# Performance work log

Hardware: AMD Instinct MI355X
Metric: run time of the kernel (lower is better)

Reference implementation:

```python
import jax, jax.numpy as jnp
import numpy as np

B, S, D = 8, 2048, 512  # batch, seq_len, dim_val == dim_attn

def setup_inputs() -> dict:
    key = jax.random.key(0)
    kx, kq, kk, kv = jax.random.split(key, 4)
    scale = 1.0 / np.sqrt(D)
    return {
        "x": jax.random.normal(kx, (B, S, D), dtype=jnp.float32),
        "Wq": jax.random.normal(kq, (D, D), dtype=jnp.float32) * scale,  # dim_input -> dim_attn
        "Wk": jax.random.normal(kk, (D, D), dtype=jnp.float32) * scale,
        "Wv": jax.random.normal(kv, (D, D), dtype=jnp.float32) * scale,  # dim_input -> dim_val
    }

def reference(x, Wq, Wk, Wv):
    # bias-free linear projections (nn.Linear stores W as [out,in]; here W is [in,out])
    Q = jnp.einsum("bsd,de->bse", x, Wq)
    K = jnp.einsum("bsd,de->bse", x, Wk)
    V = jnp.einsum("bsd,de->bse", x, Wv)
    # manual scaled dot-product attention: softmax(QK^T / sqrt(d_attn)) V
    scores = jnp.einsum("bqe,bke->bqk", Q, K) / jnp.sqrt(jnp.asarray(Q.shape[-1], Q.dtype))
    a = jax.nn.softmax(scores, axis=-1)
    return jnp.einsum("bqk,bkd->bqd", a, V)
```

## Files before the change

### kernel.cpp

```cpp
#include <hip/hip_runtime.h>


typedef __attribute__((ext_vector_type(8))) short bf16x8;
typedef __attribute__((ext_vector_type(4))) float f32x4;

__device__ __forceinline__ short f2bf(float f) {
  union { float f; unsigned u; } v; v.f = f;
  unsigned r = v.u + 0x7fffu + ((v.u >> 16) & 1u);
  return (short)(r >> 16);
}

__device__ __forceinline__ void async_cp16(const void* g, void* l) {
  __builtin_amdgcn_global_load_lds(
      (const __attribute__((address_space(1))) unsigned int*)g,
      (__attribute__((address_space(3))) unsigned int*)l, 16, 0, 0);
}

__global__ __launch_bounds__(256) void prep_kernel(const float* __restrict__ x,
                                                   const float* __restrict__ Wq,
                                                   const float* __restrict__ Wk,
                                                   const float* __restrict__ Wv,
                                                   short* __restrict__ WT,
                                                   short* __restrict__ xb) {
  if (blockIdx.x < 384) {
    int g = blockIdx.x * 256 + threadIdx.x;
    int w = g >> 15;
    int rem = g & 32767;
    int n = rem & 511;
    int k0 = (rem >> 9) << 3;
    const float* W = (w == 0) ? Wq : ((w == 1) ? Wk : Wv);
    bf16x8 o;
#pragma unroll
    for (int j = 0; j < 8; ++j) o[j] = f2bf(W[(k0 + j) * 512 + n]);
    *(bf16x8*)(WT + w * 262144 + n * 512 + k0) = o;
  } else {
    size_t g = (size_t)(blockIdx.x - 384) * 256 + threadIdx.x;
    size_t off = g * 8;
    f32x4 lo = *(const f32x4*)(x + off);
    f32x4 hi = *(const f32x4*)(x + off + 4);
    bf16x8 o;
    o[0] = f2bf(lo[0]); o[1] = f2bf(lo[1]); o[2] = f2bf(lo[2]); o[3] = f2bf(lo[3]);
    o[4] = f2bf(hi[0]); o[5] = f2bf(hi[1]); o[6] = f2bf(hi[2]); o[7] = f2bf(hi[3]);
    *(bf16x8*)(xb + off) = o;
  }
}

__global__ __launch_bounds__(256) void proj_kernel(const short* __restrict__ xb,
                                                   const short* __restrict__ WT,
                                                   short* __restrict__ QP,
                                                   short* __restrict__ KP,
                                                   short* __restrict__ VP) {
  __shared__ __align__(16) short smem[128 * 136];
  short* Af = smem;
  short* Bf = smem + 4096;
  short* Tb = smem;

  const int tid = threadIdx.x, wv = tid >> 6, ln = tid & 63;
  const int lane_m = ln & 15, lane_q = ln >> 4;
  const int z = blockIdx.z;
  const int m0 = blockIdx.x * 128, n0 = blockIdx.y * 128;
  const short* WTz = WT + z * 262144;
  const int wm = wv & 1, wn = wv >> 1;

  f32x4 zero4 = {0.f, 0.f, 0.f, 0.f};
  f32x4 acc[4][4];
#pragma unroll
  for (int i = 0; i < 4; ++i)
#pragma unroll
    for (int j = 0; j < 4; ++j) acc[i][j] = zero4;

#pragma unroll 1
  for (int kk = 0; kk < 16; ++kk) {
    const int k0 = kk * 32;
    __syncthreads();
#pragma unroll
    for (int i = 0; i < 2; ++i) {
      const int mt = wv * 2 + i;
      async_cp16(xb + (size_t)(m0 + mt * 16 + lane_m) * 512 + k0 + lane_q * 8, Af + mt * 512);
      async_cp16(WTz + (n0 + mt * 16 + lane_m) * 512 + k0 + lane_q * 8, Bf + mt * 512);
    }
    __syncthreads();
    bf16x8 a[4], b[4];
#pragma unroll
    for (int i = 0; i < 4; ++i) a[i] = *(bf16x8*)(Af + ((wm * 4 + i) * 64 + ln) * 8);
#pragma unroll
    for (int j = 0; j < 4; ++j) b[j] = *(bf16x8*)(Bf + ((wn * 4 + j) * 64 + ln) * 8);
#pragma unroll
    for (int i = 0; i < 4; ++i)
#pragma unroll
      for (int j = 0; j < 4; ++j)
        acc[i][j] = __builtin_amdgcn_mfma_f32_16x16x32_bf16(a[i], b[j], acc[i][j], 0, 0, 0);
  }
  __syncthreads();

  const int bb = m0 >> 11, ktg = (m0 & 2047) >> 6;
  if (z < 2) {
#pragma unroll
    for (int i = 0; i < 4; ++i)
#pragma unroll
      for (int j = 0; j < 4; ++j)
#pragma unroll
        for (int rr = 0; rr < 4; ++rr)
          Tb[(wm * 64 + i * 16 + lane_q * 4 + rr) * 136 + wn * 64 + j * 16 + lane_m] = f2bf(acc[i][j][rr]);
    __syncthreads();
    short* O = (z == 0) ? QP : KP;
    const int ksg0 = n0 >> 5;
#pragma unroll
    for (int p = 0; p < 8; ++p) {
      const int c2 = p * 256 + tid;
      const int ktl = c2 >> 10, wvv = (c2 >> 8) & 3, ksl = (c2 >> 6) & 3;
      const int lq = (c2 >> 4) & 3, lm = c2 & 15;
      const short* src = Tb + (ktl * 64 + wvv * 16 + lm) * 136 + ksl * 32 + lq * 8;
      size_t chunk = (size_t)bb * 131072 + (size_t)(ktg + ktl) * 4096 + wvv * 1024 +
                     (ksg0 + ksl) * 64 + lq * 16 + lm;
      *(bf16x8*)(O + chunk * 8) = *(const bf16x8*)src;
    }
  } else {
#pragma unroll
    for (int i = 0; i < 4; ++i)
#pragma unroll
      for (int j = 0; j < 4; ++j)
#pragma unroll
        for (int rr = 0; rr < 4; ++rr) {
          int rl = wm * 64 + i * 16 + lane_q * 4 + rr;
          int cl = wn * 64 + j * 16 + lane_m;
          Tb[cl * 136 + rl] = f2bf(acc[i][j][rr]);
        }
    __syncthreads();
    const int wvv = n0 >> 7;
#pragma unroll
    for (int p = 0; p < 8; ++p) {
      const int c2 = p * 256 + tid;
      const int ktl = c2 >> 10, nt = (c2 >> 7) & 7, ks2 = (c2 >> 6) & 1;
      const int lq = (c2 >> 4) & 3, lm = c2 & 15;
      const short* src = Tb + (nt * 16 + lm) * 136 + ktl * 64 + ks2 * 32 + lq * 8;
      size_t chunk = (size_t)bb * 131072 + (size_t)(ktg + ktl) * 4096 + wvv * 1024 +
                     nt * 128 + ks2 * 64 + lq * 16 + lm;
      *(bf16x8*)(VP + chunk * 8) = *(const bf16x8*)src;
    }
  }
}


#define ISSUE_K(ka0_, ka1_, ka2_, ka3_)                                      \
  asm volatile("global_load_dwordx4 %0, %16, %20\n\t"                        \
               "global_load_dwordx4 %1, %16, %20 offset:1024\n\t"            \
               "global_load_dwordx4 %2, %16, %20 offset:2048\n\t"            \
               "global_load_dwordx4 %3, %16, %20 offset:3072\n\t"            \
               "global_load_dwordx4 %4, %17, %20\n\t"                        \
               "global_load_dwordx4 %5, %17, %20 offset:1024\n\t"            \
               "global_load_dwordx4 %6, %17, %20 offset:2048\n\t"            \
               "global_load_dwordx4 %7, %17, %20 offset:3072\n\t"            \
               "global_load_dwordx4 %8, %18, %20\n\t"                        \
               "global_load_dwordx4 %9, %18, %20 offset:1024\n\t"            \
               "global_load_dwordx4 %10, %18, %20 offset:2048\n\t"           \
               "global_load_dwordx4 %11, %18, %20 offset:3072\n\t"           \
               "global_load_dwordx4 %12, %19, %20\n\t"                       \
               "global_load_dwordx4 %13, %19, %20 offset:1024\n\t"           \
               "global_load_dwordx4 %14, %19, %20 offset:2048\n\t"           \
               "global_load_dwordx4 %15, %19, %20 offset:3072\n\t"           \
               : "=&v"(kfr[0]), "=&v"(kfr[1]), "=&v"(kfr[2]), "=&v"(kfr[3]), \
                 "=&v"(kfr[4]), "=&v"(kfr[5]), "=&v"(kfr[6]), "=&v"(kfr[7]), \
                 "=&v"(kfr[8]), "=&v"(kfr[9]), "=&v"(kfr[10]), "=&v"(kfr[11]), \
                 "=&v"(kfr[12]), "=&v"(kfr[13]), "=&v"(kfr[14]), "=&v"(kfr[15]) \
               : "v"(ka0_), "v"(ka1_), "v"(ka2_), "v"(ka3_), "s"(Kp))

#define ISSUE_V0(va0_, va1_, va2_, va3_)                                     \
  asm volatile("global_load_dwordx4 %0, %8, %12\n\t"                         \
               "global_load_dwordx4 %1, %8, %12 offset:2048\n\t"             \
               "global_load_dwordx4 %2, %9, %12\n\t"                         \
               "global_load_dwordx4 %3, %9, %12 offset:2048\n\t"             \
               "global_load_dwordx4 %4, %10, %12\n\t"                        \
               "global_load_dwordx4 %5, %10, %12 offset:2048\n\t"            \
               "global_load_dwordx4 %6, %11, %12\n\t"                        \
               "global_load_dwordx4 %7, %11, %12 offset:2048\n\t"            \
               : "=&v"(bvp0[0]), "=&v"(bvp0[1]), "=&v"(bvp0[2]), "=&v"(bvp0[3]), \
                 "=&v"(bvp0[4]), "=&v"(bvp0[5]), "=&v"(bvp0[6]), "=&v"(bvp0[7]) \
               : "v"(va0_), "v"(va1_), "v"(va2_), "v"(va3_), "s"(VTp))

#define ISSUE_V1(va0_, va1_, va2_, va3_)                                     \
  asm volatile("global_load_dwordx4 %0, %8, %12 offset:1024\n\t"             \
               "global_load_dwordx4 %1, %8, %12 offset:3072\n\t"             \
               "global_load_dwordx4 %2, %9, %12 offset:1024\n\t"             \
               "global_load_dwordx4 %3, %9, %12 offset:3072\n\t"             \
               "global_load_dwordx4 %4, %10, %12 offset:1024\n\t"            \
               "global_load_dwordx4 %5, %10, %12 offset:3072\n\t"            \
               "global_load_dwordx4 %6, %11, %12 offset:1024\n\t"            \
               "global_load_dwordx4 %7, %11, %12 offset:3072\n\t"            \
               : "=&v"(bvp1[0]), "=&v"(bvp1[1]), "=&v"(bvp1[2]), "=&v"(bvp1[3]), \
                 "=&v"(bvp1[4]), "=&v"(bvp1[5]), "=&v"(bvp1[6]), "=&v"(bvp1[7]) \
               : "v"(va0_), "v"(va1_), "v"(va2_), "v"(va3_), "s"(VTp))

#define WAITK()                                                              \
  asm volatile("s_waitcnt vmcnt(8)"                                          \
               : "+v"(kfr[0]), "+v"(kfr[1]), "+v"(kfr[2]), "+v"(kfr[3]),     \
                 "+v"(kfr[4]), "+v"(kfr[5]), "+v"(kfr[6]), "+v"(kfr[7]),     \
                 "+v"(kfr[8]), "+v"(kfr[9]), "+v"(kfr[10]), "+v"(kfr[11]),   \
                 "+v"(kfr[12]), "+v"(kfr[13]), "+v"(kfr[14]), "+v"(kfr[15]))

#define WAITV()                                                              \
  asm volatile("s_waitcnt vmcnt(0)"                                          \
               : "+v"(bvp0[0]), "+v"(bvp0[1]), "+v"(bvp0[2]), "+v"(bvp0[3]), \
                 "+v"(bvp0[4]), "+v"(bvp0[5]), "+v"(bvp0[6]), "+v"(bvp0[7]), \
                 "+v"(bvp1[0]), "+v"(bvp1[1]), "+v"(bvp1[2]), "+v"(bvp1[3]), \
                 "+v"(bvp1[4]), "+v"(bvp1[5]), "+v"(bvp1[6]), "+v"(bvp1[7]))

#define DRAIN_K()                                                            \
  asm volatile("s_waitcnt vmcnt(0)"                                          \
               : "+v"(kfr[0]), "+v"(kfr[1]), "+v"(kfr[2]), "+v"(kfr[3]),     \
                 "+v"(kfr[4]), "+v"(kfr[5]), "+v"(kfr[6]), "+v"(kfr[7]),     \
                 "+v"(kfr[8]), "+v"(kfr[9]), "+v"(kfr[10]), "+v"(kfr[11]),   \
                 "+v"(kfr[12]), "+v"(kfr[13]), "+v"(kfr[14]), "+v"(kfr[15]))

__global__ __launch_bounds__(256, 2) void flash_kernel(const short* __restrict__ Q,
                                                       const short* __restrict__ K,
                                                       const short* __restrict__ VT,
                                                       float* __restrict__ out) {
  __shared__ __align__(16) short qf[16384];
  __shared__ __align__(16) short pf[4096];
  __shared__ float l_red[4][32];

  const int tid = threadIdx.x, wv = tid >> 6, ln = tid & 63;
  const int lane_m = ln & 15, lane_q = ln >> 4;
  const int b = blockIdx.x & 7, m0 = (blockIdx.x >> 3) * 32;
  const short* Qp = Q + (size_t)b * 1048576;
  const short* Kp = K + (size_t)b * 1048576;
  const short* VTp = VT + (size_t)b * 1048576;
  const float sc2 = 0.044194173824159216f * 1.4426950408889634f;

  {
    const int qt = m0 >> 6, wvm = (m0 >> 4) & 3;
#pragma unroll
    for (int r = 0; r < 8; ++r) {
      const int region = wv * 8 + r;
      const int mi = region & 1, ks = region >> 1;
      const short* src = Qp + ((size_t)(qt * 4096 + (wvm + mi) * 1024 + ks * 64) + ln) * 8;
      *(bf16x8*)(qf + (region * 64 + ln) * 8) = *(const bf16x8*)src;
    }
  }

  f32x4 zero4 = {0.f, 0.f, 0.f, 0.f};
  f32x4 O[2][8];
#pragma unroll
  for (int mi = 0; mi < 2; ++mi)
#pragma unroll
    for (int nt = 0; nt < 8; ++nt) O[mi][nt] = zero4;

  float lp[2][4] = {{0.f, 0.f, 0.f, 0.f}, {0.f, 0.f, 0.f, 0.f}};

  const unsigned kvb = (unsigned)(wv * 16384 + ln * 16);

  const int kstep = wv >> 1;
  const int quad = ((wv & 1) << 1) | (lane_m >> 3);
  const int jj = lane_m & 7;
  const int effr = ln ^ (ln >> 4);

  __syncthreads();

  bf16x8 kfr[16], bvp0[8], bvp1[8];
  ISSUE_K(kvb, kvb + 4096u, kvb + 8192u, kvb + 12288u);

#pragma unroll 1
  for (int kt = 0; kt < 32; ++kt) {
    const unsigned va0 = kvb + (unsigned)(kt * 65536);
    ISSUE_V0(va0, va0 + 4096u, va0 + 8192u, va0 + 12288u);
    WAITK();
    f32x4 s0a = zero4, s0b = zero4, s1a = zero4, s1b = zero4;
#pragma unroll
    for (int ks = 0; ks < 16; ++ks) {
      bf16x8 a0 = *(bf16x8*)(qf + ((ks * 2 + 0) * 64 + ln) * 8);
      bf16x8 a1 = *(bf16x8*)(qf + ((ks * 2 + 1) * 64 + ln) * 8);
      if (ks & 1) {
        s0b = __builtin_amdgcn_mfma_f32_16x16x32_bf16(a0, kfr[ks], s0b, 0, 0, 0);
        s1b = __builtin_amdgcn_mfma_f32_16x16x32_bf16(a1, kfr[ks], s1b, 0, 0, 0);
      } else {
        s0a = __builtin_amdgcn_mfma_f32_16x16x32_bf16(a0, kfr[ks], s0a, 0, 0, 0);
        s1a = __builtin_amdgcn_mfma_f32_16x16x32_bf16(a1, kfr[ks], s1a, 0, 0, 0);
      }
    }
    f32x4 sacc0 = s0a + s0b, sacc1 = s1a + s1b;

    ISSUE_V1(va0, va0 + 4096u, va0 + 8192u, va0 + 12288u);

    short* pfb = pf + (kt & 1) * 2048;
#pragma unroll
    for (int rr = 0; rr < 4; ++rr) {
      const int m = lane_q * 4 + rr;
      const int eff = (m ^ quad) + quad * 16;
      float p0 = exp2f(sacc0[rr] * sc2 - 12.0f);
      float p1 = exp2f(sacc1[rr] * sc2 - 12.0f);
      lp[0][rr] += p0;
      lp[1][rr] += p1;
      pfb[((kstep * 2 + 0) * 64 + eff) * 8 + jj] = f2bf(p0);
      pfb[((kstep * 2 + 1) * 64 + eff) * 8 + jj] = f2bf(p1);
    }
    __syncthreads();

    WAITV();
    bf16x8 a00 = *(bf16x8*)(pfb + (0 * 64 + effr) * 8);
    bf16x8 a01 = *(bf16x8*)(pfb + (1 * 64 + effr) * 8);
#pragma unroll
    for (int nt = 0; nt < 8; ++nt) {
      O[0][nt] = __builtin_amdgcn_mfma_f32_16x16x32_bf16(a00, bvp0[nt], O[0][nt], 0, 0, 0);
      O[1][nt] = __builtin_amdgcn_mfma_f32_16x16x32_bf16(a01, bvp0[nt], O[1][nt], 0, 0, 0);
    }
    {
      const unsigned ka0 = kvb + (unsigned)((((kt + 1) & 31)) * 65536);
      ISSUE_K(ka0, ka0 + 4096u, ka0 + 8192u, ka0 + 12288u);
    }
    bf16x8 a10 = *(bf16x8*)(pfb + (2 * 64 + effr) * 8);
    bf16x8 a11 = *(bf16x8*)(pfb + (3 * 64 + effr) * 8);
#pragma unroll
    for (int nt = 0; nt < 8; ++nt) {
      O[0][nt] = __builtin_amdgcn_mfma_f32_16x16x32_bf16(a10, bvp1[nt], O[0][nt], 0, 0, 0);
      O[1][nt] = __builtin_amdgcn_mfma_f32_16x16x32_bf16(a11, bvp1[nt], O[1][nt], 0, 0, 0);
    }
  }
  DRAIN_K();

#pragma unroll
  for (int mi = 0; mi < 2; ++mi)
#pragma unroll
    for (int rr = 0; rr < 4; ++rr) {
      float v = lp[mi][rr];
      v += __shfl_xor(v, 1);
      v += __shfl_xor(v, 2);
      v += __shfl_xor(v, 4);
      v += __shfl_xor(v, 8);
      lp[mi][rr] = v;
    }
  if (lane_m == 0) {
#pragma unroll
    for (int mi = 0; mi < 2; ++mi)
#pragma unroll
      for (int rr = 0; rr < 4; ++rr)
        l_red[wv][mi * 16 + lane_q * 4 + rr] = lp[mi][rr];
  }
  __syncthreads();

  float linv[2][4];
#pragma unroll
  for (int mi = 0; mi < 2; ++mi)
#pragma unroll
    for (int rr = 0; rr < 4; ++rr) {
      const int row = mi * 16 + lane_q * 4 + rr;
      linv[mi][rr] = 1.f / (l_red[0][row] + l_red[1][row] + l_red[2][row] + l_red[3][row]);
    }
#pragma unroll
  for (int mi = 0; mi < 2; ++mi)
#pragma unroll
    for (int nt = 0; nt < 8; ++nt)
#pragma unroll
      for (int rr = 0; rr < 4; ++rr) {
        size_t row = (size_t)b * 2048 + m0 + mi * 16 + lane_q * 4 + rr;
        out[row * 512 + wv * 128 + nt * 16 + lane_m] = O[mi][nt][rr] * linv[mi][rr];
      }
}

extern "C" void kernel_launch(void* const* d_in, const int* in_sizes, int n_in,
                              void* d_out, int out_size, void* d_ws, size_t ws_size,
                              hipStream_t stream) {
  const float* x  = (const float*)d_in[0];
  const float* Wq = (const float*)d_in[1];
  const float* Wk = (const float*)d_in[2];
  const float* Wv = (const float*)d_in[3];
  float* out = (float*)d_out;
  char* ws = (char*)d_ws;
  short* WT = (short*)ws;
  short* QP = (short*)(ws + 1572864);
  short* KP = (short*)(ws + 1572864 + 16777216);
  short* VP = (short*)(ws + 1572864 + 2 * 16777216);
  short* xb = (short*)(ws + 1572864 + 3 * 16777216);

  prep_kernel<<<dim3(384 + 4096), dim3(256), 0, stream>>>(x, Wq, Wk, Wv, WT, xb);
  proj_kernel<<<dim3(128, 4, 3), dim3(256), 0, stream>>>(xb, WT, QP, KP, VP);
  flash_kernel<<<dim3(512), dim3(256), 0, stream>>>(QP, KP, VP, out);
}
```

Measured before the change: 226.6 us.

## Enlarge flash tile to 64 query rows with 8 waves per block

```diff
diff --git a/kernel.cpp b/kernel.cpp
--- a/kernel.cpp
+++ b/kernel.cpp
@@ -167,28 +167,28 @@
 
 #define ISSUE_V0(va0_, va1_, va2_, va3_)                                     \
   asm volatile("global_load_dwordx4 %0, %8, %12\n\t"                         \
-               "global_load_dwordx4 %1, %8, %12 offset:2048\n\t"             \
+               "global_load_dwordx4 %1, %8, %12 offset:1024\n\t"             \
                "global_load_dwordx4 %2, %9, %12\n\t"                         \
-               "global_load_dwordx4 %3, %9, %12 offset:2048\n\t"             \
+               "global_load_dwordx4 %3, %9, %12 offset:1024\n\t"             \
                "global_load_dwordx4 %4, %10, %12\n\t"                        \
-               "global_load_dwordx4 %5, %10, %12 offset:2048\n\t"            \
+               "global_load_dwordx4 %5, %10, %12 offset:1024\n\t"            \
                "global_load_dwordx4 %6, %11, %12\n\t"                        \
-               "global_load_dwordx4 %7, %11, %12 offset:2048\n\t"            \
-               : "=&v"(bvp0[0]), "=&v"(bvp0[1]), "=&v"(bvp0[2]), "=&v"(bvp0[3]), \
-                 "=&v"(bvp0[4]), "=&v"(bvp0[5]), "=&v"(bvp0[6]), "=&v"(bvp0[7]) \
+               "global_load_dwordx4 %7, %11, %12 offset:1024\n\t"            \
+               : "=&v"(v0[0]), "=&v"(v0[1]), "=&v"(v0[2]), "=&v"(v0[3]),     \
+                 "=&v"(v0[4]), "=&v"(v0[5]), "=&v"(v0[6]), "=&v"(v0[7])      \
                : "v"(va0_), "v"(va1_), "v"(va2_), "v"(va3_), "s"(VTp))
 
 #define ISSUE_V1(va0_, va1_, va2_, va3_)                                     \
-  asm volatile("global_load_dwordx4 %0, %8, %12 offset:1024\n\t"             \
-               "global_load_dwordx4 %1, %8, %12 offset:3072\n\t"             \
-               "global_load_dwordx4 %2, %9, %12 offset:1024\n\t"             \
-               "global_load_dwordx4 %3, %9, %12 offset:3072\n\t"             \
-               "global_load_dwordx4 %4, %10, %12 offset:1024\n\t"            \
-               "global_load_dwordx4 %5, %10, %12 offset:3072\n\t"            \
-               "global_load_dwordx4 %6, %11, %12 offset:1024\n\t"            \
-               "global_load_dwordx4 %7, %11, %12 offset:3072\n\t"            \
-               : "=&v"(bvp1[0]), "=&v"(bvp1[1]), "=&v"(bvp1[2]), "=&v"(bvp1[3]), \
-                 "=&v"(bvp1[4]), "=&v"(bvp1[5]), "=&v"(bvp1[6]), "=&v"(bvp1[7]) \
+  asm volatile("global_load_dwordx4 %0, %8, %12\n\t"                         \
+               "global_load_dwordx4 %1, %8, %12 offset:1024\n\t"             \
+               "global_load_dwordx4 %2, %9, %12\n\t"                         \
+               "global_load_dwordx4 %3, %9, %12 offset:1024\n\t"             \
+               "global_load_dwordx4 %4, %10, %12\n\t"                        \
+               "global_load_dwordx4 %5, %10, %12 offset:1024\n\t"            \
+               "global_load_dwordx4 %6, %11, %12\n\t"                        \
+               "global_load_dwordx4 %7, %11, %12 offset:1024\n\t"            \
+               : "=&v"(v1[0]), "=&v"(v1[1]), "=&v"(v1[2]), "=&v"(v1[3]),     \
+                 "=&v"(v1[4]), "=&v"(v1[5]), "=&v"(v1[6]), "=&v"(v1[7])      \
                : "v"(va0_), "v"(va1_), "v"(va2_), "v"(va3_), "s"(VTp))
 
 #define WAITK()                                                              \
@@ -200,10 +200,10 @@
 
 #define WAITV()                                                              \
   asm volatile("s_waitcnt vmcnt(0)"                                          \
-               : "+v"(bvp0[0]), "+v"(bvp0[1]), "+v"(bvp0[2]), "+v"(bvp0[3]), \
-                 "+v"(bvp0[4]), "+v"(bvp0[5]), "+v"(bvp0[6]), "+v"(bvp0[7]), \
-                 "+v"(bvp1[0]), "+v"(bvp1[1]), "+v"(bvp1[2]), "+v"(bvp1[3]), \
-                 "+v"(bvp1[4]), "+v"(bvp1[5]), "+v"(bvp1[6]), "+v"(bvp1[7]))
+               : "+v"(v0[0]), "+v"(v0[1]), "+v"(v0[2]), "+v"(v0[3]),         \
+                 "+v"(v0[4]), "+v"(v0[5]), "+v"(v0[6]), "+v"(v0[7]),         \
+                 "+v"(v1[0]), "+v"(v1[1]), "+v"(v1[2]), "+v"(v1[3]),         \
+                 "+v"(v1[4]), "+v"(v1[5]), "+v"(v1[6]), "+v"(v1[7]))
 
 #define DRAIN_K()                                                            \
   asm volatile("s_waitcnt vmcnt(0)"                                          \
@@ -212,114 +212,120 @@
                  "+v"(kfr[8]), "+v"(kfr[9]), "+v"(kfr[10]), "+v"(kfr[11]),   \
                  "+v"(kfr[12]), "+v"(kfr[13]), "+v"(kfr[14]), "+v"(kfr[15]))
 
-__global__ __launch_bounds__(256, 2) void flash_kernel(const short* __restrict__ Q,
+#define PV_STEP(kc_, VARR)                                                     \
+  {                                                                            \
+    bf16x8 pa0 = *(bf16x8*)(pfb + (((kc_) * 4 + 0) * 64 + effr) * 8);          \
+    bf16x8 pa1 = *(bf16x8*)(pfb + (((kc_) * 4 + 1) * 64 + effr) * 8);          \
+    bf16x8 pa2 = *(bf16x8*)(pfb + (((kc_) * 4 + 2) * 64 + effr) * 8);          \
+    bf16x8 pa3 = *(bf16x8*)(pfb + (((kc_) * 4 + 3) * 64 + effr) * 8);          \
+    _Pragma("unroll")                                                          \
+    for (int ntl = 0; ntl < 4; ++ntl) {                                        \
+      bf16x8 bv = VARR[ntl * 2 + ((kc_)&1)];                                   \
+      O[0][ntl] = __builtin_amdgcn_mfma_f32_16x16x32_bf16(pa0, bv, O[0][ntl], 0, 0, 0); \
+      O[1][ntl] = __builtin_amdgcn_mfma_f32_16x16x32_bf16(pa1, bv, O[1][ntl], 0, 0, 0); \
+      O[2][ntl] = __builtin_amdgcn_mfma_f32_16x16x32_bf16(pa2, bv, O[2][ntl], 0, 0, 0); \
+      O[3][ntl] = __builtin_amdgcn_mfma_f32_16x16x32_bf16(pa3, bv, O[3][ntl], 0, 0, 0); \
+    }                                                                          \
+  }
+
+__global__ __launch_bounds__(512, 2) void flash_kernel(const short* __restrict__ Q,
                                                        const short* __restrict__ K,
                                                        const short* __restrict__ VT,
                                                        float* __restrict__ out) {
-  __shared__ __align__(16) short qf[16384];
-  __shared__ __align__(16) short pf[4096];
-  __shared__ float l_red[4][32];
-
-  const int tid = threadIdx.x, wv = tid >> 6, ln = tid & 63;
+  __shared__ __align__(16) short qf[32768];
+  __shared__ __align__(16) short pf[16384];
+  __shared__ float l_red[8][64];
+
+  const int tid = threadIdx.x, w = tid >> 6, ln = tid & 63;
   const int lane_m = ln & 15, lane_q = ln >> 4;
-  const int b = blockIdx.x & 7, m0 = (blockIdx.x >> 3) * 32;
+  const int b = blockIdx.x & 7, qt = blockIdx.x >> 3;
+  const int m0 = qt * 64;
   const short* Qp = Q + (size_t)b * 1048576;
   const short* Kp = K + (size_t)b * 1048576;
   const short* VTp = VT + (size_t)b * 1048576;
   const float sc2 = 0.044194173824159216f * 1.4426950408889634f;
 
-  {
-    const int qt = m0 >> 6, wvm = (m0 >> 4) & 3;
-#pragma unroll
-    for (int r = 0; r < 8; ++r) {
-      const int region = wv * 8 + r;
-      const int mi = region & 1, ks = region >> 1;
-      const short* src = Qp + ((size_t)(qt * 4096 + (wvm + mi) * 1024 + ks * 64) + ln) * 8;
-      *(bf16x8*)(qf + (region * 64 + ln) * 8) = *(const bf16x8*)src;
-    }
+#pragma unroll
+  for (int r = 0; r < 8; ++r) {
+    const int region = w * 8 + r;
+    const int mi = region & 3, ks = region >> 2;
+    const short* src = Qp + ((size_t)(qt * 4096 + mi * 1024 + ks * 64) + ln) * 8;
+    *(bf16x8*)(qf + (region * 64 + ln) * 8) = *(const bf16x8*)src;
   }
 
   f32x4 zero4 = {0.f, 0.f, 0.f, 0.f};
-  f32x4 O[2][8];
-#pragma unroll
-  for (int mi = 0; mi < 2; ++mi)
-#pragma unroll
-    for (int nt = 0; nt < 8; ++nt) O[mi][nt] = zero4;
-
-  float lp[2][4] = {{0.f, 0.f, 0.f, 0.f}, {0.f, 0.f, 0.f, 0.f}};
-
-  const unsigned kvb = (unsigned)(wv * 16384 + ln * 16);
-
-  const int kstep = wv >> 1;
-  const int quad = ((wv & 1) << 1) | (lane_m >> 3);
+  f32x4 O[4][4];
+#pragma unroll
+  for (int mi = 0; mi < 4; ++mi)
+#pragma unroll
+    for (int ntl = 0; ntl < 4; ++ntl) O[mi][ntl] = zero4;
+
+  float lp[4][4] = {{0.f, 0.f, 0.f, 0.f}, {0.f, 0.f, 0.f, 0.f},
+                    {0.f, 0.f, 0.f, 0.f}, {0.f, 0.f, 0.f, 0.f}};
+
+  const unsigned kvb = (unsigned)((w >> 2) * 65536 + (w & 3) * 16384 + ln * 16);
+  const unsigned vvb = (unsigned)((w >> 1) * 16384 + (w & 1) * 8192 + ln * 16);
+  const int quad = ((w & 1) << 1) | (lane_m >> 3);
   const int jj = lane_m & 7;
   const int effr = ln ^ (ln >> 4);
+  const int preg = (w >> 1) << 2;
 
   __syncthreads();
 
-  bf16x8 kfr[16], bvp0[8], bvp1[8];
+  bf16x8 kfr[16], v0[8], v1[8];
   ISSUE_K(kvb, kvb + 4096u, kvb + 8192u, kvb + 12288u);
 
 #pragma unroll 1
-  for (int kt = 0; kt < 32; ++kt) {
-    const unsigned va0 = kvb + (unsigned)(kt * 65536);
-    ISSUE_V0(va0, va0 + 4096u, va0 + 8192u, va0 + 12288u);
+  for (int kt = 0; kt < 16; ++kt) {
+    const unsigned va0 = vvb + (unsigned)(kt * 131072);
+    const unsigned va1 = va0 + 2048u, va2 = va0 + 4096u, va3 = va0 + 6144u;
+    ISSUE_V0(va0, va1, va2, va3);
     WAITK();
-    f32x4 s0a = zero4, s0b = zero4, s1a = zero4, s1b = zero4;
-#pragma unroll
-    for (int ks = 0; ks < 16; ++ks) {
-      bf16x8 a0 = *(bf16x8*)(qf + ((ks * 2 + 0) * 64 + ln) * 8);
-      bf16x8 a1 = *(bf16x8*)(qf + ((ks * 2 + 1) * 64 + ln) * 8);
-      if (ks & 1) {
-        s0b = __builtin_amdgcn_mfma_f32_16x16x32_bf16(a0, kfr[ks], s0b, 0, 0, 0);
-        s1b = __builtin_amdgcn_mfma_f32_16x16x32_bf16(a1, kfr[ks], s1b, 0, 0, 0);
-      } else {
-        s0a = __builtin_amdgcn_mfma_f32_16x16x32_bf16(a0, kfr[ks], s0a, 0, 0, 0);
-        s1a = __builtin_amdgcn_mfma_f32_16x16x32_bf16(a1, kfr[ks], s1a, 0, 0, 0);
+    f32x4 s[4] = {zero4, zero4, zero4, zero4};
+#pragma unroll
+    for (int ks = 0; ks < 12; ++ks) {
+#pragma unroll
+      for (int mi = 0; mi < 4; ++mi) {
+        bf16x8 a = *(bf16x8*)(qf + ((ks * 4 + mi) * 64 + ln) * 8);
+        s[mi] = __builtin_amdgcn_mfma_f32_16x16x32_bf16(a, kfr[ks], s[mi], 0, 0, 0);
       }
     }
-    f32x4 sacc0 = s0a + s0b, sacc1 = s1a + s1b;
-
-    ISSUE_V1(va0, va0 + 4096u, va0 + 8192u, va0 + 12288u);
-
-    short* pfb = pf + (kt & 1) * 2048;
-#pragma unroll
-    for (int rr = 0; rr < 4; ++rr) {
-      const int m = lane_q * 4 + rr;
-      const int eff = (m ^ quad) + quad * 16;
-      float p0 = exp2f(sacc0[rr] * sc2 - 12.0f);
-      float p1 = exp2f(sacc1[rr] * sc2 - 12.0f);
-      lp[0][rr] += p0;
-      lp[1][rr] += p1;
-      pfb[((kstep * 2 + 0) * 64 + eff) * 8 + jj] = f2bf(p0);
-      pfb[((kstep * 2 + 1) * 64 + eff) * 8 + jj] = f2bf(p1);
-    }
+    ISSUE_V1(va0 + 65536u, va1 + 65536u, va2 + 65536u, va3 + 65536u);
+#pragma unroll
+    for (int ks = 12; ks < 16; ++ks) {
+#pragma unroll
+      for (int mi = 0; mi < 4; ++mi) {
+        bf16x8 a = *(bf16x8*)(qf + ((ks * 4 + mi) * 64 + ln) * 8);
+        s[mi] = __builtin_amdgcn_mfma_f32_16x16x32_bf16(a, kfr[ks], s[mi], 0, 0, 0);
+      }
+    }
+    short* pfb = pf + (kt & 1) * 8192;
+#pragma unroll
+    for (int mi = 0; mi < 4; ++mi)
+#pragma unroll
+      for (int rr = 0; rr < 4; ++rr) {
+        const int m = lane_q * 4 + rr;
+        const int eff = (m ^ quad) + quad * 16;
+        float p = exp2f(s[mi][rr] * sc2 - 12.0f);
+        lp[mi][rr] += p;
+        pfb[((preg + mi) * 64 + eff) * 8 + jj] = f2bf(p);
+      }
     __syncthreads();
 
     WAITV();
-    bf16x8 a00 = *(bf16x8*)(pfb + (0 * 64 + effr) * 8);
-    bf16x8 a01 = *(bf16x8*)(pfb + (1 * 64 + effr) * 8);
-#pragma unroll
-    for (int nt = 0; nt < 8; ++nt) {
-      O[0][nt] = __builtin_amdgcn_mfma_f32_16x16x32_bf16(a00, bvp0[nt], O[0][nt], 0, 0, 0);
-      O[1][nt] = __builtin_amdgcn_mfma_f32_16x16x32_bf16(a01, bvp0[nt], O[1][nt], 0, 0, 0);
-    }
+    PV_STEP(0, v0);
     {
-      const unsigned ka0 = kvb + (unsigned)((((kt + 1) & 31)) * 65536);
+      const unsigned ka0 = kvb + (unsigned)(((kt + 1) & 15) * 131072);
       ISSUE_K(ka0, ka0 + 4096u, ka0 + 8192u, ka0 + 12288u);
     }
-    bf16x8 a10 = *(bf16x8*)(pfb + (2 * 64 + effr) * 8);
-    bf16x8 a11 = *(bf16x8*)(pfb + (3 * 64 + effr) * 8);
-#pragma unroll
-    for (int nt = 0; nt < 8; ++nt) {
-      O[0][nt] = __builtin_amdgcn_mfma_f32_16x16x32_bf16(a10, bvp1[nt], O[0][nt], 0, 0, 0);
-      O[1][nt] = __builtin_amdgcn_mfma_f32_16x16x32_bf16(a11, bvp1[nt], O[1][nt], 0, 0, 0);
-    }
+    PV_STEP(1, v0);
+    PV_STEP(2, v1);
+    PV_STEP(3, v1);
   }
   DRAIN_K();
 
 #pragma unroll
-  for (int mi = 0; mi < 2; ++mi)
+  for (int mi = 0; mi < 4; ++mi)
 #pragma unroll
     for (int rr = 0; rr < 4; ++rr) {
       float v = lp[mi][rr];
@@ -331,29 +337,32 @@
     }
   if (lane_m == 0) {
 #pragma unroll
-    for (int mi = 0; mi < 2; ++mi)
+    for (int mi = 0; mi < 4; ++mi)
 #pragma unroll
       for (int rr = 0; rr < 4; ++rr)
-        l_red[wv][mi * 16 + lane_q * 4 + rr] = lp[mi][rr];
+        l_red[w][mi * 16 + lane_q * 4 + rr] = lp[mi][rr];
   }
   __syncthreads();
 
-  float linv[2][4];
-#pragma unroll
-  for (int mi = 0; mi < 2; ++mi)
+  float linv[4][4];
+#pragma unroll
+  for (int mi = 0; mi < 4; ++mi)
 #pragma unroll
     for (int rr = 0; rr < 4; ++rr) {
       const int row = mi * 16 + lane_q * 4 + rr;
-      linv[mi][rr] = 1.f / (l_red[0][row] + l_red[1][row] + l_red[2][row] + l_red[3][row]);
-    }
-#pragma unroll
-  for (int mi = 0; mi < 2; ++mi)
-#pragma unroll
-    for (int nt = 0; nt < 8; ++nt)
+      float l = 0.f;
+#pragma unroll
+      for (int ww = 0; ww < 8; ++ww) l += l_red[ww][row];
+      linv[mi][rr] = 1.f / l;
+    }
+#pragma unroll
+  for (int mi = 0; mi < 4; ++mi)
+#pragma unroll
+    for (int ntl = 0; ntl < 4; ++ntl)
 #pragma unroll
       for (int rr = 0; rr < 4; ++rr) {
         size_t row = (size_t)b * 2048 + m0 + mi * 16 + lane_q * 4 + rr;
-        out[row * 512 + wv * 128 + nt * 16 + lane_m] = O[mi][nt][rr] * linv[mi][rr];
+        out[row * 512 + w * 64 + ntl * 16 + lane_m] = O[mi][ntl][rr] * linv[mi][rr];
       }
 }
 
@@ -374,5 +383,5 @@
 
   prep_kernel<<<dim3(384 + 4096), dim3(256), 0, stream>>>(x, Wq, Wk, Wv, WT, xb);
   proj_kernel<<<dim3(128, 4, 3), dim3(256), 0, stream>>>(xb, WT, QP, KP, VP);
-  flash_kernel<<<dim3(512), dim3(256), 0, stream>>>(QP, KP, VP, out);
-}
+  flash_kernel<<<dim3(256), dim3(512), 0, stream>>>(QP, KP, VP, out);
+}
```

Result: faster. 218.6 us (-3.5%).
